# Kernel optimization log

Hardware: AMD Instinct MI355X
Metric: run time of the kernel (lower is better)

Reference implementation:

```python
import jax, jax.numpy as jnp
import numpy as np

H = 4          # num_heads
K_HOP = 2
EPS = 1e-5


def _ln(x, g, b):
    m = jnp.mean(x, axis=-1, keepdims=True)
    v = jnp.mean((x - m) ** 2, axis=-1, keepdims=True)
    return (x - m) * jax.lax.rsqrt(v + EPS) * g + b


def setup_inputs() -> dict:
    key = jax.random.key(0)
    B, T, N, D = 16, 24, 512, 64
    F = 256
    ks = jax.random.split(key, 16)
    s = 0.02
    inp = {
        'x': jax.random.normal(ks[0], (B, T, N, D), dtype=jnp.float32),
        'adj': jax.random.uniform(ks[1], (N, N), dtype=jnp.float32),
        'Wq': jax.random.normal(ks[2], (D, D), dtype=jnp.float32) * s,
        'bq': jnp.zeros((D,), jnp.float32),
        'Wk': jax.random.normal(ks[3], (D, D), dtype=jnp.float32) * s,
        'bk': jnp.zeros((D,), jnp.float32),
        'Wv': jax.random.normal(ks[4], (D, D), dtype=jnp.float32) * s,
        'bv': jnp.zeros((D,), jnp.float32),
        'Wo': jax.random.normal(ks[5], (D, D), dtype=jnp.float32) * s,
        'bo': jnp.zeros((D,), jnp.float32),
        'gcW': jax.random.normal(ks[6], (K_HOP + 1, D, D), dtype=jnp.float32) * s,
        'gcb': jnp.zeros((K_HOP + 1, D), jnp.float32),
        'W1': jax.random.normal(ks[7], (D, F), dtype=jnp.float32) * s,
        'b1': jnp.zeros((F,), jnp.float32),
        'W2': jax.random.normal(ks[8], (F, D), dtype=jnp.float32) * s,
        'b2': jnp.zeros((D,), jnp.float32),
        'g_t': jnp.ones((D,), jnp.float32), 'b_t': jnp.zeros((D,), jnp.float32),
        'g_g': jnp.ones((D,), jnp.float32), 'b_g': jnp.zeros((D,), jnp.float32),
        'g_f': jnp.ones((D,), jnp.float32), 'b_f': jnp.zeros((D,), jnp.float32),
    }
    return inp


def _forward(x, adj, Wq, bq, Wk, bk, Wv, bv, Wo, bo, gcW, gcb,
             W1, b1, W2, b2, g_t, b_t, g_g, b_g, g_f, b_f):
    B, T, N, D = x.shape
    hd = D // H
    scale = hd ** -0.5

    # ---- temporal multi-head attention (per node, along T) ----
    def heads(y):
        return y.reshape(B, T, N, H, hd)
    q = heads(x @ Wq + bq)
    k = heads(x @ Wk + bk)
    v = heads(x @ Wv + bv)
    scores = jnp.einsum('bqnhd,bknhd->bnhqk', q, k) * scale  # [B,N,H,T,T]
    attn = jax.nn.softmax(scores, axis=-1)
    att = jnp.einsum('bnhqk,bknhd->bqnhd', attn, v).reshape(B, T, N, D)
    att = att @ Wo + bo
    h = _ln(x + att, g_t, b_t)

    # ---- K-hop graph convolution: sum_k A_hat^k X W_k ----
    A = adj + jnp.eye(N, dtype=adj.dtype)
    deg = A.sum(-1)
    dinv = jnp.clip(deg, 1e-12, None) ** -0.5
    Ahat = dinv[:, None] * A * dinv[None, :]  # [N,N], shared across B*T
    prop = h
    gout = prop @ gcW[0] + gcb[0]
    for kk in range(1, K_HOP + 1):
        prop = jnp.einsum('mn,btnd->btmd', Ahat, prop)
        gout = gout + prop @ gcW[kk] + gcb[kk]
    h = _ln(h + gout, g_g, b_g)

    # ---- FFN (exact GELU, as torch default) ----
    f = jax.nn.gelu(h @ W1 + b1, approximate=False) @ W2 + b2
    return _ln(h + f, g_f, b_f)


def reference(x, adj, Wq, bq, Wk, bk, Wv, bv, Wo, bo, gcW, gcb,
              W1, b1, W2, b2, g_t, b_t, g_g, b_g, g_f, b_f):
    return _forward(x, adj, Wq, bq, Wk, bk, Wv, bv, Wo, bo, gcW, gcb,
                    W1, b1, W2, b2, g_t, b_t, g_g, b_g, g_f, b_f)
```

## Files before the change

kernel.cpp:

```cpp
#include <hip/hip_runtime.h>
#include <hip/hip_bf16.h>
#include <math.h>

typedef __hip_bfloat16 bf16;
typedef unsigned short ushort_t;

__device__ __forceinline__ float us2f(ushort_t u){
  union { unsigned u; float f; } v; v.u = ((unsigned)u) << 16; return v.f;
}
__device__ __forceinline__ ushort_t f2us(float f){
  union { float f; unsigned u; } v; v.f = f;
  unsigned r = v.u + 0x7fff + ((v.u >> 16) & 1);
  return (ushort_t)(r >> 16);
}
__device__ __forceinline__ float ldX(float v){ return v; }
__device__ __forceinline__ float ldX(ushort_t v){ return us2f(v); }

__device__ __forceinline__ float gelu_f(float x){
  float y = x * fmaf(0.0356774081f, x*x, 0.7978845608f);
  float e = __expf(-2.0f*y);
  return x * __builtin_amdgcn_rcpf(1.0f + e);
}

#define B_ 16
#define T_ 24
#define N_ 512
#define D_ 64
#define F_ 256

typedef __attribute__((ext_vector_type(8)))  short  frag8;
typedef __attribute__((ext_vector_type(16))) float  accv16;

__device__ __forceinline__ float wave_sum(float v){
#pragma unroll
  for (int off = 32; off > 0; off >>= 1) v += __shfl_xor(v, off, 64);
  return v;
}

__global__ __launch_bounds__(64) void k_dinv(const float* __restrict__ adj,
                                             float* __restrict__ dinv){
  int m = blockIdx.x;
  float s = 0.f;
  for (int n = threadIdx.x; n < N_; n += 64) s += adj[m*N_ + n];
  s = wave_sum(s);
  if (threadIdx.x == 0){
    float deg = s + 1.0f;
    dinv[m] = rsqrtf(fmaxf(deg, 1e-12f));
  }
}

__global__ __launch_bounds__(256) void k_ahat(const float* __restrict__ adj,
                                              const float* __restrict__ dinv,
                                              ushort_t* __restrict__ AhatB){
  int idx = blockIdx.x*256 + threadIdx.x;
  int m = idx >> 9, n = idx & (N_-1);
  float a = adj[idx] + (m == n ? 1.f : 0.f);
  AhatB[idx] = f2us(dinv[m]*a*dinv[n]);
}

__global__ __launch_bounds__(256) void k_wprep(
    const float* __restrict__ W1, const float* __restrict__ W2,
    const float* __restrict__ Wq, const float* __restrict__ Wk,
    const float* __restrict__ Wv, const float* __restrict__ Wo,
    const float* __restrict__ gcW0,
    ushort_t* __restrict__ W1t, ushort_t* __restrict__ W2t,
    ushort_t* __restrict__ Wqt, ushort_t* __restrict__ Wkt,
    ushort_t* __restrict__ Wvt, ushort_t* __restrict__ Wot,
    ushort_t* __restrict__ gW0t){
  int o = blockIdx.x*256 + threadIdx.x;
  int f = o >> 6, e = o & 63;
  W1t[o] = f2us(W1[e*256 + f]);
  int d = o >> 8, e2 = o & 255;
  W2t[o] = f2us(W2[e2*64 + d]);
  if (o < 4096){
    int dd = o >> 6, ee = o & 63;
    Wqt[o] = f2us(Wq[ee*64 + dd]);
    Wkt[o] = f2us(Wk[ee*64 + dd]);
    Wvt[o] = f2us(Wv[ee*64 + dd]);
    Wot[o] = f2us(Wo[ee*64 + dd]);
    gW0t[o] = f2us(gcW0[ee*64 + dd]);
  }
}

__global__ __launch_bounds__(256, 4) void k_attn_m(
    const float* __restrict__ x,
    const ushort_t* __restrict__ Wqt, const float* __restrict__ bq,
    const ushort_t* __restrict__ Wkt, const float* __restrict__ bk,
    const ushort_t* __restrict__ Wvt, const float* __restrict__ bv,
    const ushort_t* __restrict__ Wot, const float* __restrict__ bo,
    const float* __restrict__ g_t, const float* __restrict__ b_t,
    float* __restrict__ h1)
{
  __shared__ __align__(16) char smem[37120];
  ushort_t (*xsA)[72] = (ushort_t(*)[72]) smem;
  ushort_t (*qs)[72]  = (ushort_t(*)[72])(smem + 6912);
  ushort_t (*ks)[72]  = (ushort_t(*)[72])(smem + 13824);
  float    (*Os)[65]  = (float(*)[65])   (smem + 6912);
  ushort_t *vsT       = (ushort_t*)(smem + 20736);

  int tid = threadIdx.x;
  int lane = tid & 63, w = tid >> 6;
  int l31 = lane & 31, lh = lane >> 5;
  int mt = (w >> 1) * 32, nt = (w & 1) * 32;
  int b = blockIdx.x >> 8;
  int n0 = (blockIdx.x & 255) * 2;

  {
    uint4 z4 = {0,0,0,0};
#pragma unroll
    for (int i = 0; i < 4; i++)
      *(uint4*)(smem + 20736 + (tid + i*256)*16) = z4;
  }
#pragma unroll
  for (int i = 0; i < 3; i++){
    int idx = tid + i*256;
    int row = idx >> 4, d4 = (idx & 15) * 4;
    int node = row >= 24;
    int t = row - node*24;
    const float4 v = *(const float4*)&x[(((size_t)b*T_ + t)*N_ + n0 + node)*D_ + d4];
    ushort_t tmp[4] = { f2us(v.x), f2us(v.y), f2us(v.z), f2us(v.w) };
    *(unsigned long long*)&xsA[row][d4] = *(unsigned long long*)tmp;
  }
  __syncthreads();

#pragma unroll
  for (int pj = 0; pj < 3; pj++){
    const ushort_t* Wp = (pj==0 ? Wqt : pj==1 ? Wkt : Wvt);
    accv16 a = {};
#pragma unroll
    for (int kk = 0; kk < 64; kk += 16){
      frag8 af = *(const frag8*)&xsA[mt + l31][kk + lh*8];
      frag8 bf = *(const frag8*)&Wp[(size_t)(nt + l31)*64 + kk + lh*8];
      a = __builtin_amdgcn_mfma_f32_32x32x16_bf16(af, bf, a, 0, 0, 0);
    }
    float bias = (pj==0 ? bq : pj==1 ? bk : bv)[nt + l31];
    if (pj < 2){
      ushort_t (*dst)[72] = (pj==0 ? qs : ks);
#pragma unroll
      for (int r = 0; r < 16; r++){
        int row = mt + (r & 3) + 8*(r >> 2) + 4*lh;
        if (row < 48) dst[row][nt + l31] = f2us(a[r] + bias);
      }
    } else {
      int cl = nt + l31;
      int vr0 = ((cl >> 4) << 5) + (cl & 15);
#pragma unroll
      for (int r = 0; r < 16; r++){
        int row = mt + (r & 3) + 8*(r >> 2) + 4*lh;
        if (row < 48){
          int node = (row >= 24);
          int t2 = row - node*24;
          int R = node*128 + vr0;
          vsT[R*32 + (((t2 >> 3) ^ ((R >> 1) & 3)) << 3) + (t2 & 7)] = f2us(a[r] + bias);
        }
      }
    }
  }
  __syncthreads();

  int vs_s = (l31 >> 1) & 3;
#pragma unroll
  for (int gi = 0; gi < 2; gi++){
    int g = w*2 + gi;
    int node = g >> 2, hh = g & 3;
    accv16 s = {};
    frag8 kf = *(const frag8*)&ks[node*24 + l31][hh*16 + lh*8];
    frag8 qf = *(const frag8*)&qs[node*24 + l31][hh*16 + lh*8];
    s = __builtin_amdgcn_mfma_f32_32x32x16_bf16(kf, qf, s, 0, 0, 0);
    float e[12]; float sm = 0.f;
#pragma unroll
    for (int r = 0; r < 12; r++){ e[r] = __expf(s[r]*0.25f); sm += e[r]; }
    sm += __shfl_xor(sm, 32, 64);
    float rinv = 1.0f / sm;
    union { unsigned long long q; ushort_t u[4]; } a0, a1, a2;
#pragma unroll
    for (int j = 0; j < 4; j++){
      a0.u[j] = f2us(e[j]   * rinv);
      a1.u[j] = f2us(e[4+j] * rinv);
      a2.u[j] = f2us(e[8+j] * rinv);
    }
    unsigned long long send1 = lh ? a0.q : a1.q;
    unsigned long long r1 = __shfl_xor(send1, 32, 64);
    unsigned long long r2 = __shfl_xor(a2.q, 32, 64);
    union { frag8 f; unsigned long long q[2]; } f0, f1;
    f0.q[0] = lh ? r1   : a0.q;
    f0.q[1] = lh ? a1.q : r1;
    f1.q[0] = lh ? 0ULL : a2.q;
    f1.q[1] = lh ? 0ULL : r2;
    const ushort_t* vb = &vsT[(g*32 + l31)*32];
    frag8 bf0 = *(const frag8*)&vb[((0 + lh) ^ vs_s) << 3];
    frag8 bf1 = *(const frag8*)&vb[((2 + lh) ^ vs_s) << 3];
    accv16 acc = {};
    acc = __builtin_amdgcn_mfma_f32_32x32x16_bf16(f0.f, bf0, acc, 0, 0, 0);
    acc = __builtin_amdgcn_mfma_f32_32x32x16_bf16(f1.f, bf1, acc, 0, 0, 0);
    if (l31 < 16){
#pragma unroll
      for (int r = 0; r < 12; r++){
        int row = (r & 3) + 8*(r >> 2) + 4*lh;
        xsA[node*24 + row][hh*16 + l31] = f2us(acc[r]);
      }
    }
  }
  __syncthreads();

  accv16 ao = {};
#pragma unroll
  for (int kk = 0; kk < 64; kk += 16){
    frag8 af = *(const frag8*)&xsA[mt + l31][kk + lh*8];
    frag8 bf = *(const frag8*)&Wot[(size_t)(nt + l31)*64 + kk + lh*8];
    ao = __builtin_amdgcn_mfma_f32_32x32x16_bf16(af, bf, ao, 0, 0, 0);
  }
  {
    float bov = bo[nt + l31];
#pragma unroll
    for (int r = 0; r < 16; r++){
      int row = mt + (r & 3) + 8*(r >> 2) + 4*lh;
      if (row < 48) Os[row][nt + l31] = ao[r] + bov;
    }
  }
  __syncthreads();
  {
    float gv = g_t[lane], bvv = b_t[lane];
#pragma unroll
    for (int i = 0; i < 12; i++){
      int row = w + i*4;
      int node = row >= 24;
      int t = row - node*24;
      size_t gaddr = (((size_t)b*T_ + t)*N_ + n0 + node)*D_ + lane;
      float v = Os[row][lane] + x[gaddr];
      float m = wave_sum(v) * (1.f/64.f);
      float df = v - m;
      float var = wave_sum(df*df) * (1.f/64.f);
      h1[gaddr] = df * rsqrtf(var + 1e-5f) * gv + bvv;
    }
  }
}

template<typename TX>
__global__ __launch_bounds__(256, 4) void k_prop_m(
    const ushort_t* __restrict__ Ahat,
    const TX* __restrict__ X,
    const float* __restrict__ gcWk,
    ushort_t* __restrict__ P,
    ushort_t* __restrict__ G,
    int store_p, int accum)
{
  __shared__ __align__(16) ushort_t Ab[64][72];
  __shared__ __align__(16) ushort_t Xb[64][72];
  __shared__ __align__(16) ushort_t Yt[64][72];
  __shared__ __align__(16) ushort_t Wt[64][72];
  int tid  = threadIdx.x;
  int lane = tid & 63, w = tid >> 6;
  int mw = (w >> 1) * 32, nw = (w & 1) * 32;
  int l31 = lane & 31, lh = lane >> 5;
  int m0 = blockIdx.x * 64;
  size_t slice = (size_t)blockIdx.y * (N_ * D_);
  const TX* Xg = X + slice;

  {
    int d = tid & 63, e4 = tid >> 6;
#pragma unroll
    for (int g = 0; g < 2; g++){
      int es = (e4 + g*4) * 8;
      ushort_t tmp[8];
#pragma unroll
      for (int i = 0; i < 8; i++) tmp[i] = f2us(gcWk[(es + i)*64 + d]);
      *(uint4*)&Wt[d][es] = *(uint4*)tmp;
    }
  }

  accv16 acc = {};
  int ar = tid >> 3, ac8 = (tid & 7) * 8;
  int xn = tid & 63, xk4 = tid >> 6;
  for (int k0 = 0; k0 < N_; k0 += 64){
#pragma unroll
    for (int g = 0; g < 2; g++){
      int rr = ar + g*32;
      *(uint4*)&Ab[rr][ac8] =
        *(const uint4*)&Ahat[(size_t)(m0 + rr)*N_ + k0 + ac8];
    }
#pragma unroll
    for (int g = 0; g < 2; g++){
      int ks = (xk4 + g*4) * 8;
      ushort_t tmp[8];
#pragma unroll
      for (int i = 0; i < 8; i++) tmp[i] = f2us(ldX(Xg[(size_t)(k0 + ks + i)*D_ + xn]));
      *(uint4*)&Xb[xn][ks] = *(uint4*)tmp;
    }
    __syncthreads();
#pragma unroll
    for (int kk = 0; kk < 64; kk += 16){
      frag8 af = *(const frag8*)&Ab[mw + l31][kk + lh*8];
      frag8 bf = *(const frag8*)&Xb[nw + l31][kk + lh*8];
      acc = __builtin_amdgcn_mfma_f32_32x32x16_bf16(af, bf, acc, 0, 0, 0);
    }
    __syncthreads();
  }

#pragma unroll
  for (int r = 0; r < 16; r++){
    int row = mw + (r & 3) + 8*(r >> 2) + 4*lh;
    Yt[row][nw + l31] = f2us(acc[r]);
  }
  __syncthreads();

  if (store_p){
#pragma unroll
    for (int g = 0; g < 2; g++){
      int rr = ar + g*32;
      *(uint4*)&P[slice + (size_t)(m0 + rr)*D_ + ac8] = *(const uint4*)&Yt[rr][ac8];
    }
  }

  accv16 acc2 = {};
#pragma unroll
  for (int kk = 0; kk < 64; kk += 16){
    frag8 af = *(const frag8*)&Yt[mw + l31][kk + lh*8];
    frag8 bf = *(const frag8*)&Wt[nw + l31][kk + lh*8];
    acc2 = __builtin_amdgcn_mfma_f32_32x32x16_bf16(af, bf, acc2, 0, 0, 0);
  }
#pragma unroll
  for (int r = 0; r < 16; r++){
    int row = mw + (r & 3) + 8*(r >> 2) + 4*lh;
    Ab[row][nw + l31] = f2us(acc2[r]);
  }
  __syncthreads();
#pragma unroll
  for (int g = 0; g < 2; g++){
    int rr = ar + g*32;
    uint4 vv = *(const uint4*)&Ab[rr][ac8];
    size_t base = slice + (size_t)(m0 + rr)*D_ + ac8;
    if (accum){
      uint4 ov = *(const uint4*)&G[base];
      ushort_t* s = (ushort_t*)&vv;
      ushort_t* o = (ushort_t*)&ov;
      ushort_t res[8];
#pragma unroll
      for (int i = 0; i < 8; i++) res[i] = f2us(us2f(s[i]) + us2f(o[i]));
      *(uint4*)&G[base] = *(uint4*)res;
    } else {
      *(uint4*)&G[base] = vv;
    }
  }
}

__global__ __launch_bounds__(256, 4) void k_cffn(
  const ushort_t* __restrict__ g12,
  const ushort_t* __restrict__ gW0t,
  const float* __restrict__ gcb,
  const float* __restrict__ g_g, const float* __restrict__ b_g,
  const ushort_t* __restrict__ W1t, const ushort_t* __restrict__ W2t,
  const float* __restrict__ b1, const float* __restrict__ b2,
  const float* __restrict__ g_f, const float* __restrict__ b_f,
  float* __restrict__ h)
{
  __shared__ __align__(16) char smem[26624];
  ushort_t (*hsA)[72] = (ushort_t(*)[72]) smem;
  ushort_t (*Uc)[136] = (ushort_t(*)[136])(smem + 9216);
  float    (*Sf)[68]  = (float(*)[68])    (smem + 9216);
  float    (*Os)[68]  = (float(*)[68])    (smem + 9216);

  int tid = threadIdx.x;
  int lane = tid & 63, w = tid >> 6;
  int l31 = lane & 31, lh = lane >> 5;
  size_t tok0 = (size_t)blockIdx.x * 64;

#pragma unroll
  for (int i = 0; i < 4; i++){
    int q = tid + i*256;
    int row = q >> 4, d4 = (q & 15) * 4;
    float4 v = *(const float4*)&h[tok0*64 + (size_t)q*4];
    ushort_t tmp[4] = { f2us(v.x), f2us(v.y), f2us(v.z), f2us(v.w) };
    *(unsigned long long*)&hsA[row][d4] = *(unsigned long long*)tmp;
  }
  __syncthreads();

  {
    int mg = (w >> 1) * 32, ng = (w & 1) * 32;
    accv16 ag = {};
#pragma unroll
    for (int kk = 0; kk < 64; kk += 16){
      frag8 af = *(const frag8*)&hsA[mg + l31][kk + lh*8];
      frag8 bf = *(const frag8*)&gW0t[(size_t)(ng + l31)*64 + kk + lh*8];
      ag = __builtin_amdgcn_mfma_f32_32x32x16_bf16(af, bf, ag, 0, 0, 0);
    }
    int col = ng + l31;
    float bs = gcb[col] + gcb[64 + col] + gcb[128 + col];
#pragma unroll
    for (int r = 0; r < 16; r++){
      int row = mg + (r & 3) + 8*(r >> 2) + 4*lh;
      size_t ga = (tok0 + row)*64 + col;
      Sf[row][col] = ag[r] + h[ga] + us2f(g12[ga]) + bs;
    }
  }
  __syncthreads();

  int rrow = tid >> 2, seg = (tid & 3) * 16;
  float h2r[16];
  {
    float vb[16]; float s1 = 0.f;
#pragma unroll
    for (int j4 = 0; j4 < 4; j4++){
      float4 v = *(const float4*)&Sf[rrow][seg + j4*4];
      vb[j4*4+0] = v.x; vb[j4*4+1] = v.y; vb[j4*4+2] = v.z; vb[j4*4+3] = v.w;
      s1 += v.x + v.y + v.z + v.w;
    }
    s1 += __shfl_xor(s1, 1, 64); s1 += __shfl_xor(s1, 2, 64);
    float m = s1 * (1.f/64.f);
    float s2 = 0.f;
#pragma unroll
    for (int j = 0; j < 16; j++){ vb[j] -= m; s2 += vb[j]*vb[j]; }
    s2 += __shfl_xor(s2, 1, 64); s2 += __shfl_xor(s2, 2, 64);
    float rstd = rsqrtf(s2 * (1.f/64.f) + 1e-5f);
    ushort_t tmp[16];
#pragma unroll
    for (int j4 = 0; j4 < 4; j4++){
      float4 gv = *(const float4*)&g_g[seg + j4*4];
      float4 bv = *(const float4*)&b_g[seg + j4*4];
      h2r[j4*4+0] = vb[j4*4+0]*rstd*gv.x + bv.x;
      h2r[j4*4+1] = vb[j4*4+1]*rstd*gv.y + bv.y;
      h2r[j4*4+2] = vb[j4*4+2]*rstd*gv.z + bv.z;
      h2r[j4*4+3] = vb[j4*4+3]*rstd*gv.w + bv.w;
    }
#pragma unroll
    for (int j = 0; j < 16; j++) tmp[j] = f2us(h2r[j]);
    *(uint4*)&hsA[rrow][seg]     = *(uint4*)&tmp[0];
    *(uint4*)&hsA[rrow][seg + 8] = *(uint4*)&tmp[8];
  }
  __syncthreads();

  int mw1 = (w & 1) * 32, nA = (w >> 1) * 32;
  int mw2 = (w >> 1) * 32, dw = (w & 1) * 32;
  accv16 acc2 = {};
#pragma unroll
  for (int f0 = 0; f0 < F_; f0 += 128){
    if (f0) __syncthreads();
    accv16 accA = {}, accB = {};
#pragma unroll
    for (int kk = 0; kk < 64; kk += 16){
      frag8 af  = *(const frag8*)&hsA[mw1 + l31][kk + lh*8];
      frag8 b0  = *(const frag8*)&W1t[(size_t)(f0 + nA + l31)*64 + kk + lh*8];
      frag8 b1f = *(const frag8*)&W1t[(size_t)(f0 + nA + 64 + l31)*64 + kk + lh*8];
      accA = __builtin_amdgcn_mfma_f32_32x32x16_bf16(af, b0,  accA, 0, 0, 0);
      accB = __builtin_amdgcn_mfma_f32_32x32x16_bf16(af, b1f, accB, 0, 0, 0);
    }
    {
      float bA = b1[f0 + nA + l31];
      float bB = b1[f0 + nA + 64 + l31];
#pragma unroll
      for (int r = 0; r < 16; r++){
        int row = mw1 + (r & 3) + 8*(r >> 2) + 4*lh;
        Uc[row][nA + l31]      = f2us(gelu_f(accA[r] + bA));
        Uc[row][nA + 64 + l31] = f2us(gelu_f(accB[r] + bB));
      }
    }
    __syncthreads();
#pragma unroll
    for (int kk = 0; kk < 128; kk += 16){
      frag8 af = *(const frag8*)&Uc[mw2 + l31][kk + lh*8];
      frag8 bf = *(const frag8*)&W2t[(size_t)(dw + l31)*256 + f0 + kk + lh*8];
      acc2 = __builtin_amdgcn_mfma_f32_32x32x16_bf16(af, bf, acc2, 0, 0, 0);
    }
  }
  __syncthreads();
  {
    float b2v = b2[dw + l31];
#pragma unroll
    for (int r = 0; r < 16; r++){
      int row = mw2 + (r & 3) + 8*(r >> 2) + 4*lh;
      Os[row][dw + l31] = acc2[r] + b2v;
    }
  }
  __syncthreads();

  {
    float vb[16]; float s1 = 0.f;
#pragma unroll
    for (int j4 = 0; j4 < 4; j4++){
      float4 v = *(const float4*)&Os[rrow][seg + j4*4];
      vb[j4*4+0] = v.x + h2r[j4*4+0];
      vb[j4*4+1] = v.y + h2r[j4*4+1];
      vb[j4*4+2] = v.z + h2r[j4*4+2];
      vb[j4*4+3] = v.w + h2r[j4*4+3];
      s1 += vb[j4*4+0] + vb[j4*4+1] + vb[j4*4+2] + vb[j4*4+3];
    }
    s1 += __shfl_xor(s1, 1, 64); s1 += __shfl_xor(s1, 2, 64);
    float m = s1 * (1.f/64.f);
    float s2 = 0.f;
#pragma unroll
    for (int j = 0; j < 16; j++){ vb[j] -= m; s2 += vb[j]*vb[j]; }
    s2 += __shfl_xor(s2, 1, 64); s2 += __shfl_xor(s2, 2, 64);
    float rstd = rsqrtf(s2 * (1.f/64.f) + 1e-5f);
#pragma unroll
    for (int j4 = 0; j4 < 4; j4++){
      float4 gv = *(const float4*)&g_f[seg + j4*4];
      float4 bv = *(const float4*)&b_f[seg + j4*4];
      float4 st;
      st.x = vb[j4*4+0]*rstd*gv.x + bv.x;
      st.y = vb[j4*4+1]*rstd*gv.y + bv.y;
      st.z = vb[j4*4+2]*rstd*gv.z + bv.z;
      st.w = vb[j4*4+3]*rstd*gv.w + bv.w;
      *(float4*)&h[(tok0 + rrow)*64 + seg + j4*4] = st;
    }
  }
}

extern "C" void kernel_launch(void* const* d_in, const int* in_sizes, int n_in,
                              void* d_out, int out_size, void* d_ws, size_t ws_size,
                              hipStream_t stream)
{
  const float* x   = (const float*)d_in[0];
  const float* adj = (const float*)d_in[1];
  const float* Wq  = (const float*)d_in[2];
  const float* bq  = (const float*)d_in[3];
  const float* Wk  = (const float*)d_in[4];
  const float* bk  = (const float*)d_in[5];
  const float* Wv  = (const float*)d_in[6];
  const float* bv  = (const float*)d_in[7];
  const float* Wo  = (const float*)d_in[8];
  const float* bo  = (const float*)d_in[9];
  const float* gcW = (const float*)d_in[10];
  const float* gcb = (const float*)d_in[11];
  const float* W1  = (const float*)d_in[12];
  const float* b1  = (const float*)d_in[13];
  const float* W2  = (const float*)d_in[14];
  const float* b2  = (const float*)d_in[15];
  const float* g_t = (const float*)d_in[16];
  const float* b_t = (const float*)d_in[17];
  const float* g_g = (const float*)d_in[18];
  const float* b_g = (const float*)d_in[19];
  const float* g_f = (const float*)d_in[20];
  const float* b_f = (const float*)d_in[21];

  const size_t MD = (size_t)B_*T_*N_*D_;
  float* dinv = (float*)d_ws;
  ushort_t* AhatB = (ushort_t*)(dinv + 512);
  ushort_t* p   = AhatB + (size_t)N_*N_;
  ushort_t* g12 = p + MD;
  ushort_t* W1t = g12 + MD;
  ushort_t* W2t = W1t + 256*64;
  ushort_t* Wqt = W2t + 64*256;
  ushort_t* Wkt = Wqt + 4096;
  ushort_t* Wvt = Wkt + 4096;
  ushort_t* Wot = Wvt + 4096;
  ushort_t* gW0t = Wot + 4096;
  float* h = (float*)d_out;

  k_dinv<<<N_, 64, 0, stream>>>(adj, dinv);
  k_ahat<<<(N_*N_)/256, 256, 0, stream>>>(adj, dinv, AhatB);
  k_wprep<<<64, 256, 0, stream>>>(W1, W2, Wq, Wk, Wv, Wo, gcW,
                                  W1t, W2t, Wqt, Wkt, Wvt, Wot, gW0t);
  k_attn_m<<<B_*N_/2, 256, 0, stream>>>(x, Wqt,bq, Wkt,bk, Wvt,bv, Wot,bo, g_t,b_t, h);
  k_prop_m<float><<<dim3(N_/64, B_*T_), 256, 0, stream>>>(AhatB, h, gcW + 4096, p, g12, 1, 0);
  k_prop_m<ushort_t><<<dim3(N_/64, B_*T_), 256, 0, stream>>>(AhatB, p, gcW + 8192, p, g12, 0, 1);
  k_cffn<<<(int)(MD/D_/64), 256, 0, stream>>>(g12, gW0t, gcb, g_g, b_g,
                                              W1t, W2t, b1, b2, g_f, b_f, h);
}
```

Before: 367.3 us.

## Propagate graph hops on transposed bf16 activations with pre-converted hop weights

Adds a kernel that converts the attention output to bf16 and transposes it to a per-slice [D][N] layout. The propagation kernels can then load X tiles with vectorized 16-byte reads instead of strided scalar fp32 loads plus conversion. The first hop writes its result transposed so the second hop reads the same layout. Hop weights are converted to bf16 once in the weight-prep kernel and read straight from global memory, which removes the per-block shared-memory weight staging. In exchange there is an extra kernel launch and an extra full-tensor bf16 read/write pass, and the occupancy hint rises to 5 blocks.

Result: slower. 383.0 us (+4.3%).

```diff
diff --git a/kernel.cpp b/kernel.cpp
--- a/kernel.cpp
+++ b/kernel.cpp
@@ -13,8 +13,6 @@
   unsigned r = v.u + 0x7fff + ((v.u >> 16) & 1);
   return (ushort_t)(r >> 16);
 }
-__device__ __forceinline__ float ldX(float v){ return v; }
-__device__ __forceinline__ float ldX(ushort_t v){ return us2f(v); }
 
 __device__ __forceinline__ float gelu_f(float x){
   float y = x * fmaf(0.0356774081f, x*x, 0.7978845608f);
@@ -62,11 +60,11 @@
     const float* __restrict__ W1, const float* __restrict__ W2,
     const float* __restrict__ Wq, const float* __restrict__ Wk,
     const float* __restrict__ Wv, const float* __restrict__ Wo,
-    const float* __restrict__ gcW0,
+    const float* __restrict__ gcW,
     ushort_t* __restrict__ W1t, ushort_t* __restrict__ W2t,
     ushort_t* __restrict__ Wqt, ushort_t* __restrict__ Wkt,
     ushort_t* __restrict__ Wvt, ushort_t* __restrict__ Wot,
-    ushort_t* __restrict__ gW0t){
+    ushort_t* __restrict__ gWt){
   int o = blockIdx.x*256 + threadIdx.x;
   int f = o >> 6, e = o & 63;
   W1t[o] = f2us(W1[e*256 + f]);
@@ -78,7 +76,9 @@
     Wkt[o] = f2us(Wk[ee*64 + dd]);
     Wvt[o] = f2us(Wv[ee*64 + dd]);
     Wot[o] = f2us(Wo[ee*64 + dd]);
-    gW0t[o] = f2us(gcW0[ee*64 + dd]);
+    gWt[o]        = f2us(gcW[       ee*64 + dd]);
+    gWt[4096 + o] = f2us(gcW[4096 + ee*64 + dd]);
+    gWt[8192 + o] = f2us(gcW[8192 + ee*64 + dd]);
   }
 }
 
@@ -236,56 +236,61 @@
   }
 }
 
-template<typename TX>
-__global__ __launch_bounds__(256, 4) void k_prop_m(
+__global__ __launch_bounds__(256, 8) void k_hT(const float* __restrict__ h,
+                                               ushort_t* __restrict__ hT){
+  __shared__ __align__(16) ushort_t tb[64][76];
+  int tid = threadIdx.x;
+  int n0 = (blockIdx.x & 7) * 64;
+  size_t bt = blockIdx.x >> 3;
+  const float* src = h + (bt*N_ + n0)*D_;
+#pragma unroll
+  for (int i = 0; i < 4; i++){
+    int q = tid + i*256;
+    int row = q >> 4, d4 = (q & 15)*4;
+    float4 v = *(const float4*)&src[(size_t)q*4];
+    ushort_t tmp[4] = { f2us(v.x), f2us(v.y), f2us(v.z), f2us(v.w) };
+    *(unsigned long long*)&tb[row][d4] = *(unsigned long long*)tmp;
+  }
+  __syncthreads();
+  int d = tid >> 2, nseg = (tid & 3)*16;
+  ushort_t tmp[16];
+#pragma unroll
+  for (int j = 0; j < 16; j++){
+    int jj = (j + ((d & 7) << 1)) & 15;
+    tmp[jj] = tb[nseg + jj][d];
+  }
+  ushort_t* dst = hT + (bt*D_ + d)*N_ + n0 + nseg;
+  *(uint4*)&dst[0] = *(uint4*)&tmp[0];
+  *(uint4*)&dst[8] = *(uint4*)&tmp[8];
+}
+
+__global__ __launch_bounds__(256, 5) void k_prop_m(
     const ushort_t* __restrict__ Ahat,
-    const TX* __restrict__ X,
-    const float* __restrict__ gcWk,
-    ushort_t* __restrict__ P,
+    const ushort_t* __restrict__ XT,
+    const ushort_t* __restrict__ gWkt,
+    ushort_t* __restrict__ PT,
     ushort_t* __restrict__ G,
     int store_p, int accum)
 {
   __shared__ __align__(16) ushort_t Ab[64][72];
   __shared__ __align__(16) ushort_t Xb[64][72];
   __shared__ __align__(16) ushort_t Yt[64][72];
-  __shared__ __align__(16) ushort_t Wt[64][72];
   int tid  = threadIdx.x;
   int lane = tid & 63, w = tid >> 6;
   int mw = (w >> 1) * 32, nw = (w & 1) * 32;
   int l31 = lane & 31, lh = lane >> 5;
   int m0 = blockIdx.x * 64;
   size_t slice = (size_t)blockIdx.y * (N_ * D_);
-  const TX* Xg = X + slice;
-
-  {
-    int d = tid & 63, e4 = tid >> 6;
-#pragma unroll
-    for (int g = 0; g < 2; g++){
-      int es = (e4 + g*4) * 8;
-      ushort_t tmp[8];
-#pragma unroll
-      for (int i = 0; i < 8; i++) tmp[i] = f2us(gcWk[(es + i)*64 + d]);
-      *(uint4*)&Wt[d][es] = *(uint4*)tmp;
-    }
-  }
+  const ushort_t* Xg = XT + slice;
 
   accv16 acc = {};
   int ar = tid >> 3, ac8 = (tid & 7) * 8;
-  int xn = tid & 63, xk4 = tid >> 6;
   for (int k0 = 0; k0 < N_; k0 += 64){
 #pragma unroll
     for (int g = 0; g < 2; g++){
       int rr = ar + g*32;
-      *(uint4*)&Ab[rr][ac8] =
-        *(const uint4*)&Ahat[(size_t)(m0 + rr)*N_ + k0 + ac8];
-    }
-#pragma unroll
-    for (int g = 0; g < 2; g++){
-      int ks = (xk4 + g*4) * 8;
-      ushort_t tmp[8];
-#pragma unroll
-      for (int i = 0; i < 8; i++) tmp[i] = f2us(ldX(Xg[(size_t)(k0 + ks + i)*D_ + xn]));
-      *(uint4*)&Xb[xn][ks] = *(uint4*)tmp;
+      *(uint4*)&Ab[rr][ac8] = *(const uint4*)&Ahat[(size_t)(m0 + rr)*N_ + k0 + ac8];
+      *(uint4*)&Xb[rr][ac8] = *(const uint4*)&Xg[(size_t)rr*N_ + k0 + ac8];
     }
     __syncthreads();
 #pragma unroll
@@ -305,18 +310,23 @@
   __syncthreads();
 
   if (store_p){
-#pragma unroll
-    for (int g = 0; g < 2; g++){
-      int rr = ar + g*32;
-      *(uint4*)&P[slice + (size_t)(m0 + rr)*D_ + ac8] = *(const uint4*)&Yt[rr][ac8];
-    }
+    int d = tid >> 2, mseg = (tid & 3) * 16;
+    ushort_t tmp[16];
+#pragma unroll
+    for (int j = 0; j < 16; j++){
+      int jj = (j + ((d & 7) << 1)) & 15;
+      tmp[jj] = Yt[mseg + jj][d];
+    }
+    ushort_t* dst = PT + slice + (size_t)d*N_ + m0 + mseg;
+    *(uint4*)&dst[0] = *(uint4*)&tmp[0];
+    *(uint4*)&dst[8] = *(uint4*)&tmp[8];
   }
 
   accv16 acc2 = {};
 #pragma unroll
   for (int kk = 0; kk < 64; kk += 16){
     frag8 af = *(const frag8*)&Yt[mw + l31][kk + lh*8];
-    frag8 bf = *(const frag8*)&Wt[nw + l31][kk + lh*8];
+    frag8 bf = *(const frag8*)&gWkt[(size_t)(nw + l31)*64 + kk + lh*8];
     acc2 = __builtin_amdgcn_mfma_f32_32x32x16_bf16(af, bf, acc2, 0, 0, 0);
   }
 #pragma unroll
@@ -535,24 +545,26 @@
   const size_t MD = (size_t)B_*T_*N_*D_;
   float* dinv = (float*)d_ws;
   ushort_t* AhatB = (ushort_t*)(dinv + 512);
-  ushort_t* p   = AhatB + (size_t)N_*N_;
-  ushort_t* g12 = p + MD;
-  ushort_t* W1t = g12 + MD;
+  ushort_t* PT  = AhatB + (size_t)N_*N_;
+  ushort_t* g12 = PT + MD;
+  ushort_t* hT  = g12 + MD;
+  ushort_t* W1t = hT + MD;
   ushort_t* W2t = W1t + 256*64;
   ushort_t* Wqt = W2t + 64*256;
   ushort_t* Wkt = Wqt + 4096;
   ushort_t* Wvt = Wkt + 4096;
   ushort_t* Wot = Wvt + 4096;
-  ushort_t* gW0t = Wot + 4096;
+  ushort_t* gWt = Wot + 4096;
   float* h = (float*)d_out;
 
   k_dinv<<<N_, 64, 0, stream>>>(adj, dinv);
   k_ahat<<<(N_*N_)/256, 256, 0, stream>>>(adj, dinv, AhatB);
   k_wprep<<<64, 256, 0, stream>>>(W1, W2, Wq, Wk, Wv, Wo, gcW,
-                                  W1t, W2t, Wqt, Wkt, Wvt, Wot, gW0t);
+                                  W1t, W2t, Wqt, Wkt, Wvt, Wot, gWt);
   k_attn_m<<<B_*N_/2, 256, 0, stream>>>(x, Wqt,bq, Wkt,bk, Wvt,bv, Wot,bo, g_t,b_t, h);
-  k_prop_m<float><<<dim3(N_/64, B_*T_), 256, 0, stream>>>(AhatB, h, gcW + 4096, p, g12, 1, 0);
-  k_prop_m<ushort_t><<<dim3(N_/64, B_*T_), 256, 0, stream>>>(AhatB, p, gcW + 8192, p, g12, 0, 1);
-  k_cffn<<<(int)(MD/D_/64), 256, 0, stream>>>(g12, gW0t, gcb, g_g, b_g,
+  k_hT<<<B_*T_*8, 256, 0, stream>>>(h, hT);
+  k_prop_m<<<dim3(N_/64, B_*T_), 256, 0, stream>>>(AhatB, hT, gWt + 4096, PT, g12, 1, 0);
+  k_prop_m<<<dim3(N_/64, B_*T_), 256, 0, stream>>>(AhatB, PT, gWt + 8192, PT, g12, 0, 1);
+  k_cffn<<<(int)(MD/D_/64), 256, 0, stream>>>(g12, gWt, gcb, g_g, b_g,
                                               W1t, W2t, b1, b2, g_f, b_f, h);
 }
```
